# Optimization experiments

Hardware: AMD Instinct MI355X
Metric: run time of the kernel (lower is better)

The kernel has to match this reference:

```python
import jax, jax.numpy as jnp
import numpy as np

B, S, H = 2, 2048, 1024
NH, NKV, D = 16, 8, 128
EPS = 1e-6
THETA = 1000000.0


def _rope_tables():
    inv_freq = 1.0 / (THETA ** (np.arange(0, D, 2, dtype=np.float32) / D))  # [D/2]
    pos = np.arange(S, dtype=np.float32)
    freqs = np.outer(pos, inv_freq)                 # [S, D/2]
    emb = np.concatenate([freqs, freqs], axis=-1)   # [S, D]
    cos = np.broadcast_to(np.cos(emb), (B, S, D)).copy()
    sin = np.broadcast_to(np.sin(emb), (B, S, D)).copy()
    return jnp.asarray(cos), jnp.asarray(sin)


def setup_inputs() -> dict:
    key = jax.random.key(0)
    ks = jax.random.split(key, 6)
    cos, sin = _rope_tables()
    return {
        "hidden_states": jax.random.normal(ks[0], (B, S, H), jnp.float32),
        "cos": cos,
        "sin": sin,
        "Wq": jax.random.normal(ks[1], (NH * D, H), jnp.float32) * (H ** -0.5),
        "Wk": jax.random.normal(ks[2], (NKV * D, H), jnp.float32) * (H ** -0.5),
        "Wv": jax.random.normal(ks[3], (NKV * D, H), jnp.float32) * (H ** -0.5),
        "Wo": jax.random.normal(ks[4], (H, NH * D), jnp.float32) * ((NH * D) ** -0.5),
        "q_norm_w": jnp.ones((D,), jnp.float32),
        "k_norm_w": jnp.ones((D,), jnp.float32),
    }


def _rms_norm(x, w):
    # norm over last dim (head_dim), computed in fp32
    var = jnp.mean(x.astype(jnp.float32) ** 2, axis=-1, keepdims=True)
    return w * (x * jax.lax.rsqrt(var + EPS))


def _rotate_half(x):
    x1, x2 = jnp.split(x, 2, axis=-1)
    return jnp.concatenate([-x2, x1], axis=-1)


def reference(hidden_states, cos, sin, Wq, Wk, Wv, Wo, q_norm_w, k_norm_w):
    b, s, _ = hidden_states.shape
    # projections -> [B, n_heads, S, D]
    q = (hidden_states @ Wq.T).reshape(b, s, NH, D)
    k = (hidden_states @ Wk.T).reshape(b, s, NKV, D)
    v = (hidden_states @ Wv.T).reshape(b, s, NKV, D)
    q = _rms_norm(q, q_norm_w).transpose(0, 2, 1, 3)   # [B,NH,S,D]
    k = _rms_norm(k, k_norm_w).transpose(0, 2, 1, 3)   # [B,NKV,S,D]
    v = v.transpose(0, 2, 1, 3)                        # [B,NKV,S,D]
    # RoPE (cos/sin: [B,S,D] -> broadcast over heads)
    c = cos[:, None, :, :]
    sn = sin[:, None, :, :]
    q = q * c + _rotate_half(q) * sn
    k = k * c + _rotate_half(k) * sn
    # repeat_kv for GQA
    n_rep = NH // NKV
    k = jnp.repeat(k, n_rep, axis=1)                   # [B,NH,S,D]
    v = jnp.repeat(v, n_rep, axis=1)
    scale = D ** -0.5
    scores = jnp.einsum('bhqd,bhkd->bhqk', q, k) * scale
    causal = jnp.tril(jnp.ones((s, s), bool))
    scores = jnp.where(causal[None, None], scores, -jnp.inf)
    attn = jax.nn.softmax(scores.astype(jnp.float32), axis=-1)
    out = jnp.einsum('bhqk,bhkd->bhqd', attn, v)       # [B,NH,S,D]
    out = out.transpose(0, 2, 1, 3).reshape(b, s, NH * D)
    return out @ Wo.T                                  # [B,S,H]
```

## Files before the change

### kernel.cpp

```cpp
#include <hip/hip_runtime.h>
#include <hip/hip_bf16.h>
#include <stdint.h>

#define BB 2
#define SS 2048
#define HH 1024
#define NHEAD 16
#define NKVH 8
#define DD 128
#define MM (BB*SS)

typedef __bf16 bf16_t;
typedef __bf16 bf16x8 __attribute__((ext_vector_type(8)));
typedef __bf16 bf16x4 __attribute__((ext_vector_type(4)));
typedef float  f32x4  __attribute__((ext_vector_type(4)));

__global__ __launch_bounds__(256) void k_cvt(const float* __restrict__ in,
                                             bf16_t* __restrict__ out, int n4) {
  int i = blockIdx.x * 256 + threadIdx.x;
  const int stride = gridDim.x * 256;
  for (; i < n4; i += stride) {
    float4 v = reinterpret_cast<const float4*>(in)[i];
    bf16x4 o;
    o[0] = (bf16_t)v.x; o[1] = (bf16_t)v.y; o[2] = (bf16_t)v.z; o[3] = (bf16_t)v.w;
    reinterpret_cast<bf16x4*>(out)[i] = o;
  }
}

template <typename CT>
__global__ __launch_bounds__(256, 3) void k_gemm_lds(
    const bf16_t* __restrict__ A, const bf16_t* __restrict__ Bm,
    CT* __restrict__ C, int M, int N, int K) {
  __shared__ bf16_t As[128 * 64];
  __shared__ bf16_t Bs[128 * 64];
  const int t = threadIdx.x;
  const int lane = t & 63, wave = t >> 6;
  const int c = lane & 15, g = lane >> 4;
  const int wm = wave >> 1, wn = wave & 1;
  const long m0 = (long)blockIdx.y * 128;
  const long n0 = (long)blockIdx.x * 128;
  const int srow = t >> 3, sc8 = t & 7;

  const bf16_t* Ag = A + (m0 + srow) * K + sc8 * 8;
  const bf16_t* Bg = Bm + (n0 + srow) * K + sc8 * 8;

  f32x4 acc[4][4] = {};
  const int nk = K >> 6;
  for (int kt = 0; kt < nk; ++kt) {
    const long koff = (long)kt * 64;
    __syncthreads();
#pragma unroll
    for (int i = 0; i < 4; ++i) {
      __builtin_amdgcn_global_load_lds(
          (const __attribute__((address_space(1))) uint32_t*)(const void*)(Ag + (long)i * 32 * K + koff),
          (__attribute__((address_space(3))) uint32_t*)(void*)(&As[(i * 256 + t) * 8]),
          16, 0, 0);
      __builtin_amdgcn_global_load_lds(
          (const __attribute__((address_space(1))) uint32_t*)(const void*)(Bg + (long)i * 32 * K + koff),
          (__attribute__((address_space(3))) uint32_t*)(void*)(&Bs[(i * 256 + t) * 8]),
          16, 0, 0);
    }
    __syncthreads();
#pragma unroll
    for (int kk = 0; kk < 2; ++kk) {
      bf16x8 af[4], bfr[4];
#pragma unroll
      for (int mi = 0; mi < 4; ++mi)
        af[mi] = *reinterpret_cast<const bf16x8*>(
            &As[(wm * 64 + mi * 16 + c) * 64 + kk * 32 + g * 8]);
#pragma unroll
      for (int ni = 0; ni < 4; ++ni)
        bfr[ni] = *reinterpret_cast<const bf16x8*>(
            &Bs[(wn * 64 + ni * 16 + c) * 64 + kk * 32 + g * 8]);
#pragma unroll
      for (int mi = 0; mi < 4; ++mi)
#pragma unroll
        for (int ni = 0; ni < 4; ++ni)
          acc[mi][ni] = __builtin_amdgcn_mfma_f32_16x16x32_bf16(
              af[mi], bfr[ni], acc[mi][ni], 0, 0, 0);
    }
  }
#pragma unroll
  for (int mi = 0; mi < 4; ++mi)
#pragma unroll
    for (int ni = 0; ni < 4; ++ni)
#pragma unroll
      for (int r = 0; r < 4; ++r) {
        long m = m0 + wm * 64 + mi * 16 + 4 * g + r;
        long n = n0 + wn * 64 + ni * 16 + c;
        C[m * N + n] = (CT)acc[mi][ni][r];
      }
}

template <int DO_NR>
__global__ __launch_bounds__(256) void k_nr(
    const bf16_t* __restrict__ raw, bf16_t* __restrict__ outp,
    const float* __restrict__ w, const float* __restrict__ cosb,
    const float* __restrict__ sinb, int nheads, int rstride) {
  const int wid = (blockIdx.x * 256 + threadIdx.x) >> 6;
  const int lane = threadIdx.x & 63;
  const int h = wid % nheads;
  const int bs = wid / nheads;
  const int b = bs / SS, s = bs - b * SS;
  const bf16_t* rp = raw + (long)bs * rstride + h * DD;
  float x0 = (float)rp[lane];
  float x1 = (float)rp[lane + 64];
  bf16_t o0, o1;
  if (DO_NR) {
    float ssq = x0 * x0 + x1 * x1;
#pragma unroll
    for (int m = 1; m < 64; m <<= 1) ssq += __shfl_xor(ssq, m);
    const float rs = rsqrtf(ssq * (1.0f / DD) + 1e-6f);
    const float xn0 = x0 * rs * w[lane];
    const float xn1 = x1 * rs * w[lane + 64];
    const float cc = cosb[(long)bs * DD + lane];
    const float sn = sinb[(long)bs * DD + lane];
    o0 = (bf16_t)(xn0 * cc - xn1 * sn);
    o1 = (bf16_t)(xn1 * cc + xn0 * sn);
  } else {
    o0 = (bf16_t)x0; o1 = (bf16_t)x1;
  }
  bf16_t* op = outp + (((long)b * nheads + h) * SS + s) * DD;
  op[lane] = o0;
  op[lane + 64] = o1;
}

__global__ __launch_bounds__(256, 2) void k_attn(
    const bf16_t* __restrict__ Qh, const bf16_t* __restrict__ Kh,
    const bf16_t* __restrict__ Vh, bf16_t* __restrict__ AO) {
  __shared__ bf16_t Ks[64 * 128];
  __shared__ bf16_t Vs[128 * 66];
  __shared__ bf16_t Pq[4 * 2 * 16 * 64];
  const int t = threadIdx.x;
  const int lane = t & 63, wave = t >> 6;
  const int c = lane & 15, g = lane >> 4;

  const int id = blockIdx.x;
  const int xcd = id & 7, j2 = (id >> 3) & 3, qt8 = (id >> 5) & 7, half = id >> 8;
  const int qt = half ? (15 - qt8) : qt8;
  const int hb = xcd * 4 + j2;
  const int h = hb & 15, b = hb >> 4;
  const int kvh = h >> 1;

  const int qbase = qt * 128 + wave * 32;
  const int qg0 = qbase + c, qg1 = qbase + 16 + c;

  const bf16_t* qp = Qh + (((long)b * NHEAD + h) * SS) * DD;
  bf16x8 qf[2][4];
#pragma unroll
  for (int qc = 0; qc < 2; ++qc)
#pragma unroll
    for (int kb = 0; kb < 4; ++kb)
      qf[qc][kb] = *reinterpret_cast<const bf16x8*>(
          qp + (long)(qbase + qc * 16 + c) * DD + kb * 32 + g * 8);

  const bf16_t* kp = Kh + ((long)b * NKVH + kvh) * SS * DD;
  const bf16_t* vp = Vh + ((long)b * NKVH + kvh) * SS * DD;

  f32x4 o[8][2] = {};
  float mrow[2] = {-1e30f, -1e30f}, lrow[2] = {0.f, 0.f};
  const int srow2 = t >> 4, sc16 = t & 15;
  const int kv_end = qt * 128 + 128;
  const float scale = 0.08838834764831845f;
  const int c7x8 = 8 * (c & 7);
  unsigned short* Vsu = reinterpret_cast<unsigned short*>(Vs);

  for (int kv0 = 0; kv0 < kv_end; kv0 += 64) {
    __syncthreads();
#pragma unroll
    for (int rr = 0; rr < 4; ++rr) {
      const int row = srow2 + rr * 16;
      uint4 kvv = *reinterpret_cast<const uint4*>(kp + (long)(kv0 + row) * DD + sc16 * 8);
      *reinterpret_cast<uint4*>(&Ks[row * 128 + 8 * (sc16 ^ (row & 7))]) = kvv;
      uint4 vvv = *reinterpret_cast<const uint4*>(vp + (long)(kv0 + row) * DD + sc16 * 8);
      unsigned int vw[4] = {vvv.x, vvv.y, vvv.z, vvv.w};
#pragma unroll
      for (int j = 0; j < 4; ++j) {
        Vsu[(sc16 * 8 + 2 * j) * 66 + row]     = (unsigned short)(vw[j] & 0xffffu);
        Vsu[(sc16 * 8 + 2 * j + 1) * 66 + row] = (unsigned short)(vw[j] >> 16);
      }
    }
    __syncthreads();

    if (kv0 <= qbase + 31) {
      f32x4 s[2][4] = {};
#pragma unroll
      for (int kb = 0; kb < 4; ++kb) {
        bf16x8 kf[4];
#pragma unroll
        for (int kc = 0; kc < 4; ++kc)
          kf[kc] = *reinterpret_cast<const bf16x8*>(
              &Ks[(kc * 16 + c) * 128 + 8 * (((kb << 2) | g) ^ (c & 7))]);
#pragma unroll
        for (int qc = 0; qc < 2; ++qc)
#pragma unroll
          for (int kc = 0; kc < 4; ++kc)
            s[qc][kc] = __builtin_amdgcn_mfma_f32_16x16x32_bf16(
                kf[kc], qf[qc][kb], s[qc][kc], 0, 0, 0);
      }
#pragma unroll
      for (int qc = 0; qc < 2; ++qc) {
        const int qg = qc ? qg1 : qg0;
        float sv[16];
#pragma unroll
        for (int i = 0; i < 16; ++i) {
          const int key = kv0 + (i >> 2) * 16 + 4 * g + (i & 3);
          const float x = s[qc][i >> 2][i & 3];
          sv[i] = (key <= qg) ? x * scale : -1e30f;
        }
        float vm = sv[0];
#pragma unroll
        for (int i = 1; i < 16; ++i) vm = fmaxf(vm, sv[i]);
        vm = fmaxf(vm, __shfl_xor(vm, 16));
        vm = fmaxf(vm, __shfl_xor(vm, 32));
        const float mnew = fmaxf(mrow[qc], vm);
        const float alpha = __expf(mrow[qc] - mnew);
        float p[16], ps = 0.f;
#pragma unroll
        for (int i = 0; i < 16; ++i) { p[i] = __expf(sv[i] - mnew); ps += p[i]; }
        ps += __shfl_xor(ps, 16);
        ps += __shfl_xor(ps, 32);
        lrow[qc] = lrow[qc] * alpha + ps;
        mrow[qc] = mnew;
#pragma unroll
        for (int dt = 0; dt < 8; ++dt) o[dt][qc] = o[dt][qc] * alpha;
#pragma unroll
        for (int kc = 0; kc < 4; ++kc) {
          bf16x4 pk;
#pragma unroll
          for (int r = 0; r < 4; ++r) pk[r] = (bf16_t)p[kc * 4 + r];
          *reinterpret_cast<bf16x4*>(
              &Pq[((wave * 2 + qc) * 16 + c) * 64 + ((kc * 16 + 4 * g) ^ c7x8)]) = pk;
        }
      }
#pragma unroll
      for (int kc2 = 0; kc2 < 2; ++kc2) {
        bf16x8 pf[2];
#pragma unroll
        for (int qc = 0; qc < 2; ++qc)
          pf[qc] = *reinterpret_cast<const bf16x8*>(
              &Pq[((wave * 2 + qc) * 16 + c) * 64 + ((kc2 * 32 + g * 8) ^ c7x8)]);
#pragma unroll
        for (int dt = 0; dt < 8; ++dt) {
          const int eb = (dt * 16 + c) * 66 + kc2 * 32 + g * 8;
          union { uint32_t u[4]; bf16x8 v; } vu;
          const uint32_t* vsrc = reinterpret_cast<const uint32_t*>(&Vs[eb]);
          vu.u[0] = vsrc[0]; vu.u[1] = vsrc[1];
          vu.u[2] = vsrc[2]; vu.u[3] = vsrc[3];
#pragma unroll
          for (int qc = 0; qc < 2; ++qc)
            o[dt][qc] = __builtin_amdgcn_mfma_f32_16x16x32_bf16(
                vu.v, pf[qc], o[dt][qc], 0, 0, 0);
        }
      }
    }
  }
#pragma unroll
  for (int qc = 0; qc < 2; ++qc) {
    const float linv = 1.0f / lrow[qc];
    bf16_t* aop = AO + ((long)(b * SS) + qbase + qc * 16 + c) * (NHEAD * DD) + h * DD;
#pragma unroll
    for (int dt = 0; dt < 8; ++dt) {
      bf16x4 ov;
#pragma unroll
      for (int r = 0; r < 4; ++r) ov[r] = (bf16_t)(o[dt][qc][r] * linv);
      *reinterpret_cast<bf16x4*>(aop + dt * 16 + 4 * g) = ov;
    }
  }
}

extern "C" void kernel_launch(void* const* d_in, const int* in_sizes, int n_in,
                              void* d_out, int out_size, void* d_ws, size_t ws_size,
                              hipStream_t stream) {
  const float* hidden = (const float*)d_in[0];
  const float* cosb   = (const float*)d_in[1];
  const float* sinb   = (const float*)d_in[2];
  const float* Wq     = (const float*)d_in[3];
  const float* Wk     = (const float*)d_in[4];
  const float* Wv     = (const float*)d_in[5];
  const float* Wo     = (const float*)d_in[6];
  const float* qnw    = (const float*)d_in[7];
  const float* knw    = (const float*)d_in[8];
  float* outp = (float*)d_out;
  char* ws = (char*)d_ws;
  const size_t MB = 1024 * 1024;
  bf16_t* hbf   = (bf16_t*)(ws + 0);
  bf16_t* wqkv  = (bf16_t*)(ws + 8 * MB);
  bf16_t* wob   = (bf16_t*)(ws + 16 * MB);
  bf16_t* qkvr  = (bf16_t*)(ws + 20 * MB);
  bf16_t* qn    = (bf16_t*)(ws + 52 * MB);
  bf16_t* kn    = (bf16_t*)(ws + 68 * MB);
  bf16_t* vn    = (bf16_t*)(ws + 76 * MB);
  bf16_t* ao    = qkvr;

  k_cvt<<<2048, 256, 0, stream>>>(hidden, hbf, MM * HH / 4);
  k_cvt<<<1024, 256, 0, stream>>>(Wq, wqkv, 2048 * HH / 4);
  k_cvt<<<512, 256, 0, stream>>>(Wk, wqkv + 2048 * HH, 1024 * HH / 4);
  k_cvt<<<512, 256, 0, stream>>>(Wv, wqkv + 3072 * HH, 1024 * HH / 4);
  k_cvt<<<1024, 256, 0, stream>>>(Wo, wob, HH * NHEAD * DD / 4);

  k_gemm_lds<bf16_t><<<dim3(32, 32), 256, 0, stream>>>(hbf, wqkv, qkvr, MM, 4096, 1024);

  k_nr<1><<<MM * NHEAD / 4, 256, 0, stream>>>(qkvr, qn, qnw, cosb, sinb, NHEAD, 4096);
  k_nr<1><<<MM * NKVH / 4, 256, 0, stream>>>(qkvr + 2048, kn, knw, cosb, sinb, NKVH, 4096);
  k_nr<0><<<MM * NKVH / 4, 256, 0, stream>>>(qkvr + 3072, vn, knw, cosb, sinb, NKVH, 4096);

  k_attn<<<dim3(512), 256, 0, stream>>>(qn, kn, vn, ao);

  k_gemm_lds<float><<<dim3(8, 32), 256, 0, stream>>>(ao, wob, outp, MM, 1024, 2048);
}
```

Baseline: 309.3 us.

## Pre-transpose V, merge fp32-to-bf16 conversions, split-K output GEMM with atomics

V is now transposed into a [D,S] buffer by a dedicated kernel, so the attention kernel loads V tiles with vector copies into a swizzled LDS layout. This replaces the per-element 16-bit scatter stores used before. The five conversion launches are merged into one kernel. The output projection is split along K into two slices that accumulate into a zeroed fp32 output with atomicAdd, which doubles its grid. The trade-off is an extra zeroing pass and atomic traffic, and the float sum order is no longer deterministic.

```diff
diff --git a/kernel.cpp b/kernel.cpp
--- a/kernel.cpp
+++ b/kernel.cpp
@@ -15,22 +15,38 @@
 typedef __bf16 bf16x4 __attribute__((ext_vector_type(4)));
 typedef float  f32x4  __attribute__((ext_vector_type(4)));
 
-__global__ __launch_bounds__(256) void k_cvt(const float* __restrict__ in,
-                                             bf16_t* __restrict__ out, int n4) {
+__global__ __launch_bounds__(256) void k_cvt_all(
+    const float* __restrict__ h, const float* __restrict__ wq,
+    const float* __restrict__ wk, const float* __restrict__ wv,
+    const float* __restrict__ wo, bf16_t* __restrict__ hbf,
+    bf16_t* __restrict__ wqkv, bf16_t* __restrict__ wob) {
   int i = blockIdx.x * 256 + threadIdx.x;
   const int stride = gridDim.x * 256;
-  for (; i < n4; i += stride) {
-    float4 v = reinterpret_cast<const float4*>(in)[i];
+  for (; i < 2621440; i += stride) {
+    const float* src; bf16_t* dst; int off;
+    if (i < 1048576)      { src = h;  dst = hbf;            off = i; }
+    else if (i < 1572864) { src = wq; dst = wqkv;           off = i - 1048576; }
+    else if (i < 1835008) { src = wk; dst = wqkv + 2097152; off = i - 1572864; }
+    else if (i < 2097152) { src = wv; dst = wqkv + 3145728; off = i - 1835008; }
+    else                  { src = wo; dst = wob;            off = i - 2097152; }
+    float4 v = reinterpret_cast<const float4*>(src)[off];
     bf16x4 o;
     o[0] = (bf16_t)v.x; o[1] = (bf16_t)v.y; o[2] = (bf16_t)v.z; o[3] = (bf16_t)v.w;
-    reinterpret_cast<bf16x4*>(out)[i] = o;
-  }
-}
-
-template <typename CT>
+    reinterpret_cast<bf16x4*>(dst)[off] = o;
+  }
+}
+
+__global__ __launch_bounds__(256) void k_zero(float4* __restrict__ p, int n4) {
+  int i = blockIdx.x * 256 + threadIdx.x;
+  const int stride = gridDim.x * 256;
+  const float4 z = make_float4(0.f, 0.f, 0.f, 0.f);
+  for (; i < n4; i += stride) p[i] = z;
+}
+
+template <typename CT, int ATOM>
 __global__ __launch_bounds__(256, 3) void k_gemm_lds(
     const bf16_t* __restrict__ A, const bf16_t* __restrict__ Bm,
-    CT* __restrict__ C, int M, int N, int K) {
+    CT* __restrict__ C, int M, int N, int LD, int Ksplit) {
   __shared__ bf16_t As[128 * 64];
   __shared__ bf16_t Bs[128 * 64];
   const int t = threadIdx.x;
@@ -39,24 +55,25 @@
   const int wm = wave >> 1, wn = wave & 1;
   const long m0 = (long)blockIdx.y * 128;
   const long n0 = (long)blockIdx.x * 128;
+  const long kbase = (long)blockIdx.z * Ksplit;
   const int srow = t >> 3, sc8 = t & 7;
 
-  const bf16_t* Ag = A + (m0 + srow) * K + sc8 * 8;
-  const bf16_t* Bg = Bm + (n0 + srow) * K + sc8 * 8;
+  const bf16_t* Ag = A + (m0 + srow) * LD + kbase + sc8 * 8;
+  const bf16_t* Bg = Bm + (n0 + srow) * LD + kbase + sc8 * 8;
 
   f32x4 acc[4][4] = {};
-  const int nk = K >> 6;
+  const int nk = Ksplit >> 6;
   for (int kt = 0; kt < nk; ++kt) {
     const long koff = (long)kt * 64;
     __syncthreads();
 #pragma unroll
     for (int i = 0; i < 4; ++i) {
       __builtin_amdgcn_global_load_lds(
-          (const __attribute__((address_space(1))) uint32_t*)(const void*)(Ag + (long)i * 32 * K + koff),
+          (const __attribute__((address_space(1))) uint32_t*)(const void*)(Ag + (long)i * 32 * LD + koff),
           (__attribute__((address_space(3))) uint32_t*)(void*)(&As[(i * 256 + t) * 8]),
           16, 0, 0);
       __builtin_amdgcn_global_load_lds(
-          (const __attribute__((address_space(1))) uint32_t*)(const void*)(Bg + (long)i * 32 * K + koff),
+          (const __attribute__((address_space(1))) uint32_t*)(const void*)(Bg + (long)i * 32 * LD + koff),
           (__attribute__((address_space(3))) uint32_t*)(void*)(&Bs[(i * 256 + t) * 8]),
           16, 0, 0);
     }
@@ -88,11 +105,11 @@
       for (int r = 0; r < 4; ++r) {
         long m = m0 + wm * 64 + mi * 16 + 4 * g + r;
         long n = n0 + wn * 64 + ni * 16 + c;
-        C[m * N + n] = (CT)acc[mi][ni][r];
+        if (ATOM) atomicAdd((float*)&C[m * N + n], acc[mi][ni][r]);
+        else      C[m * N + n] = (CT)acc[mi][ni][r];
       }
 }
 
-template <int DO_NR>
 __global__ __launch_bounds__(256) void k_nr(
     const bf16_t* __restrict__ raw, bf16_t* __restrict__ outp,
     const float* __restrict__ w, const float* __restrict__ cosb,
@@ -105,31 +122,52 @@
   const bf16_t* rp = raw + (long)bs * rstride + h * DD;
   float x0 = (float)rp[lane];
   float x1 = (float)rp[lane + 64];
-  bf16_t o0, o1;
-  if (DO_NR) {
-    float ssq = x0 * x0 + x1 * x1;
-#pragma unroll
-    for (int m = 1; m < 64; m <<= 1) ssq += __shfl_xor(ssq, m);
-    const float rs = rsqrtf(ssq * (1.0f / DD) + 1e-6f);
-    const float xn0 = x0 * rs * w[lane];
-    const float xn1 = x1 * rs * w[lane + 64];
-    const float cc = cosb[(long)bs * DD + lane];
-    const float sn = sinb[(long)bs * DD + lane];
-    o0 = (bf16_t)(xn0 * cc - xn1 * sn);
-    o1 = (bf16_t)(xn1 * cc + xn0 * sn);
-  } else {
-    o0 = (bf16_t)x0; o1 = (bf16_t)x1;
-  }
+  float ssq = x0 * x0 + x1 * x1;
+#pragma unroll
+  for (int m = 1; m < 64; m <<= 1) ssq += __shfl_xor(ssq, m);
+  const float rs = rsqrtf(ssq * (1.0f / DD) + 1e-6f);
+  const float xn0 = x0 * rs * w[lane];
+  const float xn1 = x1 * rs * w[lane + 64];
+  const float cc = cosb[(long)bs * DD + lane];
+  const float sn = sinb[(long)bs * DD + lane];
+  bf16_t o0 = (bf16_t)(xn0 * cc - xn1 * sn);
+  bf16_t o1 = (bf16_t)(xn1 * cc + xn0 * sn);
   bf16_t* op = outp + (((long)b * nheads + h) * SS + s) * DD;
   op[lane] = o0;
   op[lane + 64] = o1;
 }
 
+__global__ __launch_bounds__(256) void k_vt(const bf16_t* __restrict__ src,
+                                            bf16_t* __restrict__ vt) {
+  __shared__ bf16_t Ls[64 * 136];
+  const int t = threadIdx.x;
+  const int s0 = blockIdx.x * 64;
+  const int kvh = blockIdx.y;
+  const int b = blockIdx.z;
+  const bf16_t* ip = src + ((long)b * SS) * 4096 + 3072 + kvh * DD;
+#pragma unroll
+  for (int i = 0; i < 4; ++i) {
+    const int cid = i * 256 + t;
+    const int sr = cid >> 4, c8 = cid & 15;
+    *reinterpret_cast<uint4*>(&Ls[sr * 136 + c8 * 8]) =
+        *reinterpret_cast<const uint4*>(ip + (long)(s0 + sr) * 4096 + c8 * 8);
+  }
+  __syncthreads();
+  const int d = t >> 1, sh = (t & 1) * 32;
+  bf16_t* op = vt + (((long)b * NKVH + kvh) * DD + d) * SS + s0 + sh;
+  bf16_t buf[32];
+#pragma unroll
+  for (int j = 0; j < 32; ++j) buf[j] = Ls[(sh + j) * 136 + d];
+#pragma unroll
+  for (int q = 0; q < 4; ++q)
+    reinterpret_cast<uint4*>(op)[q] = reinterpret_cast<uint4*>(buf)[q];
+}
+
 __global__ __launch_bounds__(256, 2) void k_attn(
     const bf16_t* __restrict__ Qh, const bf16_t* __restrict__ Kh,
-    const bf16_t* __restrict__ Vh, bf16_t* __restrict__ AO) {
+    const bf16_t* __restrict__ VT, bf16_t* __restrict__ AO) {
   __shared__ bf16_t Ks[64 * 128];
-  __shared__ bf16_t Vs[128 * 66];
+  __shared__ bf16_t Vs[128 * 64];
   __shared__ bf16_t Pq[4 * 2 * 16 * 64];
   const int t = threadIdx.x;
   const int lane = t & 63, wave = t >> 6;
@@ -155,7 +193,7 @@
           qp + (long)(qbase + qc * 16 + c) * DD + kb * 32 + g * 8);
 
   const bf16_t* kp = Kh + ((long)b * NKVH + kvh) * SS * DD;
-  const bf16_t* vp = Vh + ((long)b * NKVH + kvh) * SS * DD;
+  const bf16_t* vtp = VT + ((long)b * NKVH + kvh) * DD * SS;
 
   f32x4 o[8][2] = {};
   float mrow[2] = {-1e30f, -1e30f}, lrow[2] = {0.f, 0.f};
@@ -163,7 +201,6 @@
   const int kv_end = qt * 128 + 128;
   const float scale = 0.08838834764831845f;
   const int c7x8 = 8 * (c & 7);
-  unsigned short* Vsu = reinterpret_cast<unsigned short*>(Vs);
 
   for (int kv0 = 0; kv0 < kv_end; kv0 += 64) {
     __syncthreads();
@@ -172,13 +209,13 @@
       const int row = srow2 + rr * 16;
       uint4 kvv = *reinterpret_cast<const uint4*>(kp + (long)(kv0 + row) * DD + sc16 * 8);
       *reinterpret_cast<uint4*>(&Ks[row * 128 + 8 * (sc16 ^ (row & 7))]) = kvv;
-      uint4 vvv = *reinterpret_cast<const uint4*>(vp + (long)(kv0 + row) * DD + sc16 * 8);
-      unsigned int vw[4] = {vvv.x, vvv.y, vvv.z, vvv.w};
-#pragma unroll
-      for (int j = 0; j < 4; ++j) {
-        Vsu[(sc16 * 8 + 2 * j) * 66 + row]     = (unsigned short)(vw[j] & 0xffffu);
-        Vsu[(sc16 * 8 + 2 * j + 1) * 66 + row] = (unsigned short)(vw[j] >> 16);
-      }
+    }
+#pragma unroll
+    for (int i = 0; i < 4; ++i) {
+      const int cid = i * 256 + t;
+      const int d = cid >> 3, c8 = cid & 7;
+      uint4 vv = *reinterpret_cast<const uint4*>(vtp + (long)d * SS + kv0 + c8 * 8);
+      *reinterpret_cast<uint4*>(&Vs[d * 64 + 8 * (c8 ^ (d & 7))]) = vv;
     }
     __syncthreads();
 
@@ -242,15 +279,13 @@
               &Pq[((wave * 2 + qc) * 16 + c) * 64 + ((kc2 * 32 + g * 8) ^ c7x8)]);
 #pragma unroll
         for (int dt = 0; dt < 8; ++dt) {
-          const int eb = (dt * 16 + c) * 66 + kc2 * 32 + g * 8;
-          union { uint32_t u[4]; bf16x8 v; } vu;
-          const uint32_t* vsrc = reinterpret_cast<const uint32_t*>(&Vs[eb]);
-          vu.u[0] = vsrc[0]; vu.u[1] = vsrc[1];
-          vu.u[2] = vsrc[2]; vu.u[3] = vsrc[3];
+          const int dr = dt * 16 + c;
+          bf16x8 vf = *reinterpret_cast<const bf16x8*>(
+              &Vs[dr * 64 + 8 * ((kc2 * 4 + g) ^ (c & 7))]);
 #pragma unroll
           for (int qc = 0; qc < 2; ++qc)
             o[dt][qc] = __builtin_amdgcn_mfma_f32_16x16x32_bf16(
-                vu.v, pf[qc], o[dt][qc], 0, 0, 0);
+                vf, pf[qc], o[dt][qc], 0, 0, 0);
         }
       }
     }
@@ -290,22 +325,21 @@
   bf16_t* qkvr  = (bf16_t*)(ws + 20 * MB);
   bf16_t* qn    = (bf16_t*)(ws + 52 * MB);
   bf16_t* kn    = (bf16_t*)(ws + 68 * MB);
-  bf16_t* vn    = (bf16_t*)(ws + 76 * MB);
+  bf16_t* vt    = (bf16_t*)(ws + 76 * MB);
   bf16_t* ao    = qkvr;
 
-  k_cvt<<<2048, 256, 0, stream>>>(hidden, hbf, MM * HH / 4);
-  k_cvt<<<1024, 256, 0, stream>>>(Wq, wqkv, 2048 * HH / 4);
-  k_cvt<<<512, 256, 0, stream>>>(Wk, wqkv + 2048 * HH, 1024 * HH / 4);
-  k_cvt<<<512, 256, 0, stream>>>(Wv, wqkv + 3072 * HH, 1024 * HH / 4);
-  k_cvt<<<1024, 256, 0, stream>>>(Wo, wob, HH * NHEAD * DD / 4);
-
-  k_gemm_lds<bf16_t><<<dim3(32, 32), 256, 0, stream>>>(hbf, wqkv, qkvr, MM, 4096, 1024);
-
-  k_nr<1><<<MM * NHEAD / 4, 256, 0, stream>>>(qkvr, qn, qnw, cosb, sinb, NHEAD, 4096);
-  k_nr<1><<<MM * NKVH / 4, 256, 0, stream>>>(qkvr + 2048, kn, knw, cosb, sinb, NKVH, 4096);
-  k_nr<0><<<MM * NKVH / 4, 256, 0, stream>>>(qkvr + 3072, vn, knw, cosb, sinb, NKVH, 4096);
-
-  k_attn<<<dim3(512), 256, 0, stream>>>(qn, kn, vn, ao);
-
-  k_gemm_lds<float><<<dim3(8, 32), 256, 0, stream>>>(ao, wob, outp, MM, 1024, 2048);
-}
+  k_cvt_all<<<2048, 256, 0, stream>>>(hidden, Wq, Wk, Wv, Wo, hbf, wqkv, wob);
+
+  k_gemm_lds<bf16_t, 0><<<dim3(32, 32, 1), 256, 0, stream>>>(
+      hbf, wqkv, qkvr, MM, 4096, 1024, 1024);
+
+  k_nr<<<MM * NHEAD / 4, 256, 0, stream>>>(qkvr, qn, qnw, cosb, sinb, NHEAD, 4096);
+  k_nr<<<MM * NKVH / 4, 256, 0, stream>>>(qkvr + 2048, kn, knw, cosb, sinb, NKVH, 4096);
+  k_vt<<<dim3(32, 8, 2), 256, 0, stream>>>(qkvr, vt);
+
+  k_attn<<<dim3(512), 256, 0, stream>>>(qn, kn, vt, ao);
+
+  k_zero<<<1024, 256, 0, stream>>>((float4*)outp, MM * 1024 / 4);
+  k_gemm_lds<float, 1><<<dim3(8, 32, 2), 256, 0, stream>>>(
+      ao, wob, outp, MM, 1024, 2048, 1024);
+}
```

Measured after the change: 348.9 us. 1.13x slower.
